# Optimization experiments

Measured on AMD Instinct MI355X. Metric: run time of the kernel, lower is better.

Reference implementation:

```python
import jax, jax.numpy as jnp
import numpy as np

B, L, D, DIN, S, R, K = 2, 1024, 1024, 2048, 16, 64, 4


def setup_inputs() -> dict:
    key = jax.random.key(0)
    ks = jax.random.split(key, 8)
    f = lambda k, sh, sc: jax.random.normal(k, sh, jnp.float32) * sc
    return {
        "x": f(ks[0], (B, L, D), 1.0),
        "norm_w": jnp.ones((D,), jnp.float32),
        "W_in": f(ks[1], (D, 2 * DIN), D ** -0.5),
        "conv_w": f(ks[2], (DIN, 1, K), 0.5),
        "conv_b": jnp.zeros((DIN,), jnp.float32),
        "W_x": f(ks[3], (DIN, R + 2 * S), DIN ** -0.5),
        "W_dt": f(ks[4], (R, DIN), R ** -0.5),
        "b_dt": f(ks[5], (DIN,), 0.1),
        "A_log": jnp.log(jnp.broadcast_to(jnp.arange(1, S + 1, dtype=jnp.float32), (DIN, S))),
        "D_skip": jnp.ones((DIN,), jnp.float32),
        "W_out": f(ks[6], (DIN, D), DIN ** -0.5),
    }


def reference(x, norm_w, W_in, conv_w, conv_b, W_x, W_dt, b_dt, A_log, D_skip, W_out):
    eps = 1e-5
    # RMSNorm
    xn = x * jax.lax.rsqrt(jnp.mean(x * x, axis=-1, keepdims=True) + eps) * norm_w
    # input projection -> (x_branch, gate)
    xz = xn @ W_in                       # [B,L,2*DIN]
    xi, z = jnp.split(xz, 2, axis=-1)
    # causal depthwise conv1d along L
    xt = jnp.transpose(xi, (0, 2, 1))    # [B,DIN,L]
    xc = jax.lax.conv_general_dilated(xt, conv_w, (1,), [(K - 1, 0)],
                                      feature_group_count=DIN)
    xc = jnp.transpose(xc, (0, 2, 1)) + conv_b
    xc = jax.nn.silu(xc)                 # [B,L,DIN]
    # input-dependent SSM parameters
    xd = xc @ W_x                        # [B,L,R+2S]
    dt, Bm, Cm = jnp.split(xd, [R, R + S], axis=-1)
    dt = jax.nn.softplus(dt @ W_dt + b_dt)           # [B,L,DIN]
    A = -jnp.exp(A_log)                              # [DIN,S]
    dA = jnp.exp(dt[..., None] * A)                  # [B,L,DIN,S]
    dBu = (dt * xc)[..., None] * Bm[:, :, None, :]   # [B,L,DIN,S]
    # selective scan: h_t = dA_t * h_{t-1} + dBu_t (parallel associative scan)
    def comb(c1, c2):
        a1, b1 = c1
        a2, b2 = c2
        return a1 * a2, a2 * b1 + b2
    _, h = jax.lax.associative_scan(comb, (dA, dBu), axis=1)
    y = jnp.einsum('blds,bls->bld', h, Cm) + D_skip * xc
    y = y * jax.nn.silu(z)
    return x + y @ W_out
```

## Files before the change

### kernel.cpp

```cpp
#include <hip/hip_runtime.h>

#define B_    2
#define L_    1024
#define D_    1024
#define DIN_  2048
#define S_    16
#define R_    64
#define NTOK  (B_ * L_)
#define NCH   32
#define LC    (L_ / NCH)

typedef unsigned short u16;
typedef short bf16x8 __attribute__((ext_vector_type(8)));
typedef float f32x4  __attribute__((ext_vector_type(4)));

__device__ __forceinline__ u16 f2bf(float f) {
    union { float f; unsigned u; } v; v.f = f;
    return (u16)((v.u + 0x7FFFu + ((v.u >> 16) & 1u)) >> 16);
}
__device__ __forceinline__ float bf2f(u16 b) {
    union { unsigned u; float f; } v; v.u = (unsigned)b << 16;
    return v.f;
}

__global__ __launch_bounds__(256) void rmsnorm_kernel(
    const float* __restrict__ x, const float* __restrict__ w, u16* __restrict__ xn) {
    int row = blockIdx.x;
    const float4 v = ((const float4*)(x + (size_t)row * D_))[threadIdx.x];
    float ss = v.x * v.x + v.y * v.y + v.z * v.z + v.w * v.w;
#pragma unroll
    for (int o = 32; o > 0; o >>= 1) ss += __shfl_down(ss, o);
    __shared__ float red[4];
    if ((threadIdx.x & 63) == 0) red[threadIdx.x >> 6] = ss;
    __syncthreads();
    float tot = red[0] + red[1] + red[2] + red[3];
    float sc = rsqrtf(tot * (1.f / (float)D_) + 1e-5f);
    const float4 wv = ((const float4*)w)[threadIdx.x];
    ushort4 o;
    o.x = f2bf(v.x * sc * wv.x);
    o.y = f2bf(v.y * sc * wv.y);
    o.z = f2bf(v.z * sc * wv.z);
    o.w = f2bf(v.w * sc * wv.w);
    ((ushort4*)(xn + (size_t)row * D_))[threadIdx.x] = o;
}

__device__ __forceinline__ void transp_tile(
    const float* __restrict__ src, u16* __restrict__ dst,
    int R, int Csrc, int cx, int cy, int tx, int ty) {
    __shared__ float tile[32][33];
    int c0 = cx * 32, r0 = cy * 32;
#pragma unroll
    for (int i = 0; i < 32; i += 8)
        tile[ty + i][tx] = (c0 + tx < Csrc)
            ? src[(size_t)(r0 + ty + i) * Csrc + c0 + tx] : 0.f;
    __syncthreads();
#pragma unroll
    for (int i = 0; i < 32; i += 8)
        dst[(size_t)(c0 + ty + i) * R + r0 + tx] = f2bf(tile[tx][ty + i]);
}

__global__ __launch_bounds__(256) void transpose_all_kernel(
    const float* __restrict__ W_in,  u16* __restrict__ WinT,
    const float* __restrict__ W_out, u16* __restrict__ WoutT,
    const float* __restrict__ W_x,   u16* __restrict__ WxT,
    const float* __restrict__ W_dt,  u16* __restrict__ WdtT) {
    int bid = blockIdx.x;
    int tx = threadIdx.x & 31, ty = threadIdx.x >> 5;
    if (bid < 4096) {
        transp_tile(W_in, WinT, D_, 2 * DIN_, bid % 128, bid / 128, tx, ty);
    } else if (bid < 6144) {
        int b = bid - 4096;
        transp_tile(W_out, WoutT, DIN_, D_, b % 32, b / 32, tx, ty);
    } else if (bid < 6400) {
        int b = bid - 6144;
        transp_tile(W_x, WxT, DIN_, 96, b % 4, b / 4, tx, ty);
    } else {
        int b = bid - 6400;
        transp_tile(W_dt, WdtT, R_, DIN_, b % 64, b / 64, tx, ty);
    }
}

#define BK 64
template<int BM, int BN>
__global__ __launch_bounds__(256) void gemm_bf16(
    const u16* __restrict__ A, int lda,
    const u16* __restrict__ Bt, int ldb,
    float* __restrict__ C, u16* __restrict__ Cbf, int ldc,
    const float* __restrict__ aux,
    int M, int N, int K, int mode) {
    constexpr int WGM = (BM >= 128) ? 2 : 1;
    constexpr int WGN = 4 / WGM;
    constexpr int FM = BM / (16 * WGM);
    constexpr int FN = BN / (16 * WGN);
    constexpr int ABYTES = BM * BK * 2;
    constexpr int BBYTES = BN * BK * 2;
    __shared__ __align__(16) u16 As[2][BM * BK];
    __shared__ __align__(16) u16 Bs[2][BN * BK];
    const int t = threadIdx.x;
    const int w = t >> 6;
    const int l = t & 63;
    const int lr = l & 15;
    const int kg = l >> 4;
    const int wm = (w / WGN) * (BM / WGM);
    const int wn = (w % WGN) * (BN / WGN);

    int nwg = gridDim.x * gridDim.y * gridDim.z;
    int flat = blockIdx.x + gridDim.x * (blockIdx.y + gridDim.y * blockIdx.z);
    int swz = (flat & 7) * (nwg >> 3) + (flat >> 3);
    int bx = swz % gridDim.x;
    int rem = swz / gridDim.x;
    int by = rem % gridDim.y;
    int bz = rem / gridDim.y;

    const int row0 = by * BM;
    const int col0 = bx * BN;
    const int kbase = bz * K;

    auto stage = [&](int buf, int k0) {
#pragma unroll
        for (int i = 0; i < ABYTES; i += 4096) {
            int off = i + t * 16;
            int grow = off >> 7;
            int sw = ((off >> 4) & 7) ^ (grow & 7);
            const u16* ga = A + (size_t)(row0 + grow) * lda + k0 + sw * 8;
            __builtin_amdgcn_global_load_lds(
                (const __attribute__((address_space(1))) unsigned int*)(const void*)ga,
                (__attribute__((address_space(3))) unsigned int*)(void*)&As[buf][off >> 1],
                16, 0, 0);
        }
#pragma unroll
        for (int i = 0; i < BBYTES; i += 4096) {
            int off = i + t * 16;
            int grow = off >> 7;
            int sw = ((off >> 4) & 7) ^ (grow & 7);
            const u16* gb = Bt + (size_t)(col0 + grow) * ldb + k0 + sw * 8;
            __builtin_amdgcn_global_load_lds(
                (const __attribute__((address_space(1))) unsigned int*)(const void*)gb,
                (__attribute__((address_space(3))) unsigned int*)(void*)&Bs[buf][off >> 1],
                16, 0, 0);
        }
    };

    f32x4 acc[FM][FN];
#pragma unroll
    for (int i = 0; i < FM; ++i)
#pragma unroll
        for (int j = 0; j < FN; ++j) acc[i][j] = (f32x4){0.f, 0.f, 0.f, 0.f};

    const int nt = K / BK;
    stage(0, kbase);
    asm volatile("s_waitcnt vmcnt(0)" ::: "memory");
    __builtin_amdgcn_s_barrier();
    asm volatile("" ::: "memory");

    int cur = 0;
    for (int tt = 0; tt < nt; ++tt) {
        if (tt + 1 < nt) stage(cur ^ 1, kbase + (tt + 1) * BK);
#pragma unroll
        for (int ks = 0; ks < 2; ++ks) {
            bf16x8 af[FM], bfr[FN];
#pragma unroll
            for (int mt = 0; mt < FM; ++mt) {
                int ar = wm + mt * 16 + lr;
                af[mt] = *(const bf16x8*)&As[cur][ar * 64 + (((ks << 2) | kg) ^ (ar & 7)) * 8];
            }
#pragma unroll
            for (int nt2 = 0; nt2 < FN; ++nt2) {
                int br = wn + nt2 * 16 + lr;
                bfr[nt2] = *(const bf16x8*)&Bs[cur][br * 64 + (((ks << 2) | kg) ^ (br & 7)) * 8];
            }
            __builtin_amdgcn_s_setprio(1);
#pragma unroll
            for (int mt = 0; mt < FM; ++mt)
#pragma unroll
                for (int nt2 = 0; nt2 < FN; ++nt2)
                    acc[mt][nt2] = __builtin_amdgcn_mfma_f32_16x16x32_bf16(
                        af[mt], bfr[nt2], acc[mt][nt2], 0, 0, 0);
            __builtin_amdgcn_s_setprio(0);
        }
        if (tt + 1 < nt) {
            asm volatile("s_waitcnt vmcnt(0)" ::: "memory");
            __builtin_amdgcn_s_barrier();
            asm volatile("" ::: "memory");
        }
        cur ^= 1;
    }

    size_t pbase = (mode == 3) ? (size_t)bz * M * N : 0;
#pragma unroll
    for (int mt = 0; mt < FM; ++mt) {
#pragma unroll
        for (int nt2 = 0; nt2 < FN; ++nt2) {
#pragma unroll
            for (int r = 0; r < 4; ++r) {
                int row = row0 + wm + mt * 16 + kg * 4 + r;
                int col = col0 + wn + nt2 * 16 + lr;
                float v = acc[mt][nt2][r];
                if (mode == 1) { v += aux[col]; v = (v > 20.f) ? v : log1pf(__expf(v)); }
                else if (mode == 2) { v += aux[(size_t)row * ldc + col]; }
                if (C)   C[pbase + (size_t)row * ldc + col] = v;
                if (Cbf) Cbf[(size_t)row * ldc + col] = f2bf(v);
            }
        }
    }
}

__global__ __launch_bounds__(256) void reduce_wx_kernel(
    const float* __restrict__ part, float* __restrict__ xd, u16* __restrict__ xdb) {
    int i = blockIdx.x * 256 + threadIdx.x;
    float4 s = ((const float4*)part)[i];
#pragma unroll
    for (int k = 1; k < 16; ++k) {
        float4 v = ((const float4*)(part + (size_t)k * NTOK * 128))[i];
        s.x += v.x; s.y += v.y; s.z += v.z; s.w += v.w;
    }
    ((float4*)xd)[i] = s;
    ushort4 o; o.x = f2bf(s.x); o.y = f2bf(s.y); o.z = f2bf(s.z); o.w = f2bf(s.w);
    ((ushort4*)xdb)[i] = o;
}

__global__ __launch_bounds__(256) void reduce_out_kernel(
    const float* __restrict__ part, const float* __restrict__ x, float* __restrict__ out) {
    int i = blockIdx.x * 256 + threadIdx.x;
    float4 s = ((const float4*)part)[i];
#pragma unroll
    for (int k = 1; k < 4; ++k) {
        float4 v = ((const float4*)(part + (size_t)k * NTOK * D_))[i];
        s.x += v.x; s.y += v.y; s.z += v.z; s.w += v.w;
    }
    float4 xv = ((const float4*)x)[i];
    s.x += xv.x; s.y += xv.y; s.z += xv.z; s.w += xv.w;
    ((float4*)out)[i] = s;
}

__global__ __launch_bounds__(256) void conv_silu_kernel(
    const float* __restrict__ xz, const float* __restrict__ cw,
    const float* __restrict__ cb, u16* __restrict__ xcb) {
    size_t idx = (size_t)blockIdx.x * 256 + threadIdx.x;
    int c = (int)(idx & (DIN_ - 1));
    int g = (int)(idx >> 11);
    int bl0 = g * 4;
    int l0 = bl0 & (L_ - 1);
    const float4 w = ((const float4*)cw)[c];
    float bias = cb[c];
    float v[7];
#pragma unroll
    for (int k = 0; k < 7; ++k) {
        int off = k - 3;
        v[k] = (l0 + off >= 0) ? xz[(size_t)(bl0 + off) * 4096 + c] : 0.f;
    }
#pragma unroll
    for (int j = 0; j < 4; ++j) {
        float acc = bias + v[j] * w.x + v[j + 1] * w.y + v[j + 2] * w.z + v[j + 3] * w.w;
        float s = acc / (1.f + __expf(-acc));
        xcb[(size_t)(bl0 + j) * DIN_ + c] = f2bf(s);
    }
}

__global__ __launch_bounds__(256) void scan_chunk_kernel(
    const float* __restrict__ dt, const u16* __restrict__ xcb,
    const float* __restrict__ xd, const float* __restrict__ A_log,
    float* __restrict__ Pout, float* __restrict__ Hout) {
    int din = blockIdx.x * 256 + threadIdx.x;
    int c = blockIdx.y, b = blockIdx.z;
    float a[S_], h[S_];
#pragma unroll
    for (int q = 0; q < 4; ++q) {
        float4 av = ((const float4*)(A_log + (size_t)din * S_))[q];
        a[q * 4 + 0] = -__expf(av.x); a[q * 4 + 1] = -__expf(av.y);
        a[q * 4 + 2] = -__expf(av.z); a[q * 4 + 3] = -__expf(av.w);
    }
#pragma unroll
    for (int s = 0; s < S_; ++s) h[s] = 0.f;
    float sdt = 0.f;
    size_t rbase = (size_t)b * L_ + (size_t)c * LC;
#pragma unroll 2
    for (int i = 0; i < LC; ++i) {
        size_t row = rbase + i;
        float dtv = dt[row * DIN_ + din];
        float xcv = bf2f(xcb[row * DIN_ + din]);
        float du = dtv * xcv;
        sdt += dtv;
        const float4* bp = (const float4*)(xd + row * 128 + 64);
        float4 B0 = bp[0], B1 = bp[1], B2 = bp[2], B3 = bp[3];
        float Bv[S_] = {B0.x, B0.y, B0.z, B0.w, B1.x, B1.y, B1.z, B1.w,
                        B2.x, B2.y, B2.z, B2.w, B3.x, B3.y, B3.z, B3.w};
#pragma unroll
        for (int s = 0; s < S_; ++s) {
            float dA = __expf(dtv * a[s]);
            h[s] = h[s] * dA + du * Bv[s];
        }
    }
    size_t obase = ((size_t)(b * NCH + c) * DIN_ + din) * S_;
#pragma unroll
    for (int q = 0; q < 4; ++q) {
        float4 pv, hv;
        pv.x = __expf(a[q * 4 + 0] * sdt); pv.y = __expf(a[q * 4 + 1] * sdt);
        pv.z = __expf(a[q * 4 + 2] * sdt); pv.w = __expf(a[q * 4 + 3] * sdt);
        hv.x = h[q * 4 + 0]; hv.y = h[q * 4 + 1]; hv.z = h[q * 4 + 2]; hv.w = h[q * 4 + 3];
        ((float4*)(Pout + obase))[q] = pv;
        ((float4*)(Hout + obase))[q] = hv;
    }
}

__global__ __launch_bounds__(256) void scan_combine_kernel(
    const float* __restrict__ P, const float* __restrict__ H,
    float* __restrict__ h0) {
    int tid = blockIdx.x * 256 + threadIdx.x;
    int ds = tid & (DIN_ * S_ - 1);
    int b = tid >> 15;
    float h = 0.f;
#pragma unroll
    for (int c = 0; c < NCH; ++c) {
        size_t idx = ((size_t)(b * NCH + c) * DIN_ * S_) + ds;
        h0[idx] = h;
        h = H[idx] + P[idx] * h;
    }
}

__global__ __launch_bounds__(256) void scan_final_kernel(
    const float* __restrict__ dt, const u16* __restrict__ xcb,
    const float* __restrict__ xd, const float* __restrict__ A_log,
    const float* __restrict__ h0, const float* __restrict__ Dskip,
    const float* __restrict__ xz, u16* __restrict__ yg) {
    int din = blockIdx.x * 256 + threadIdx.x;
    int c = blockIdx.y, b = blockIdx.z;
    float a[S_], h[S_];
#pragma unroll
    for (int q = 0; q < 4; ++q) {
        float4 av = ((const float4*)(A_log + (size_t)din * S_))[q];
        a[q * 4 + 0] = -__expf(av.x); a[q * 4 + 1] = -__expf(av.y);
        a[q * 4 + 2] = -__expf(av.z); a[q * 4 + 3] = -__expf(av.w);
    }
    size_t ibase = ((size_t)(b * NCH + c) * DIN_ + din) * S_;
#pragma unroll
    for (int q = 0; q < 4; ++q) {
        float4 hv = ((const float4*)(h0 + ibase))[q];
        h[q * 4 + 0] = hv.x; h[q * 4 + 1] = hv.y; h[q * 4 + 2] = hv.z; h[q * 4 + 3] = hv.w;
    }
    float dsk = Dskip[din];
    size_t rbase = (size_t)b * L_ + (size_t)c * LC;
#pragma unroll 2
    for (int i = 0; i < LC; ++i) {
        size_t row = rbase + i;
        float dtv = dt[row * DIN_ + din];
        float xcv = bf2f(xcb[row * DIN_ + din]);
        float du = dtv * xcv;
        const float4* bp = (const float4*)(xd + row * 128 + 64);
        float4 B0 = bp[0], B1 = bp[1], B2 = bp[2], B3 = bp[3];
        const float4* cp = (const float4*)(xd + row * 128 + 80);
        float4 C0 = cp[0], C1 = cp[1], C2 = cp[2], C3 = cp[3];
        float Bv[S_] = {B0.x, B0.y, B0.z, B0.w, B1.x, B1.y, B1.z, B1.w,
                        B2.x, B2.y, B2.z, B2.w, B3.x, B3.y, B3.z, B3.w};
        float Cv[S_] = {C0.x, C0.y, C0.z, C0.w, C1.x, C1.y, C1.z, C1.w,
                        C2.x, C2.y, C2.z, C2.w, C3.x, C3.y, C3.z, C3.w};
        float py = 0.f;
#pragma unroll
        for (int s = 0; s < S_; ++s) {
            float dA = __expf(dtv * a[s]);
            h[s] = h[s] * dA + du * Bv[s];
            py += h[s] * Cv[s];
        }
        float zv = xz[row * 4096 + DIN_ + din];
        float y = (py + dsk * xcv) * (zv / (1.f + __expf(-zv)));
        yg[row * DIN_ + din] = f2bf(y);
    }
}

extern "C" void kernel_launch(void* const* d_in, const int* in_sizes, int n_in,
                              void* d_out, int out_size, void* d_ws, size_t ws_size,
                              hipStream_t stream) {
    const float* x      = (const float*)d_in[0];
    const float* norm_w = (const float*)d_in[1];
    const float* W_in   = (const float*)d_in[2];
    const float* conv_w = (const float*)d_in[3];
    const float* conv_b = (const float*)d_in[4];
    const float* W_x    = (const float*)d_in[5];
    const float* W_dt   = (const float*)d_in[6];
    const float* b_dt   = (const float*)d_in[7];
    const float* A_log  = (const float*)d_in[8];
    const float* D_skip = (const float*)d_in[9];
    const float* W_out  = (const float*)d_in[10];
    float* out = (float*)d_out;

    char* p = (char*)d_ws;
    auto alloc = [&](size_t bytes) {
        char* r = p;
        p += (bytes + 255) & ~(size_t)255;
        return r;
    };
    u16*   xn    = (u16*)alloc((size_t)NTOK * D_ * 2);
    u16*   WinT  = (u16*)alloc((size_t)2 * DIN_ * D_ * 2);
    u16*   WoutT = (u16*)alloc((size_t)D_ * DIN_ * 2);
    u16*   WxT   = (u16*)alloc((size_t)128 * DIN_ * 2);
    u16*   WdtT  = (u16*)alloc((size_t)DIN_ * R_ * 2);
    float* xz    = (float*)alloc((size_t)NTOK * 2 * DIN_ * 4);
    u16*   xcb   = (u16*)alloc((size_t)NTOK * DIN_ * 2);
    float* xd    = (float*)alloc((size_t)NTOK * 128 * 4);
    u16*   xdb   = (u16*)alloc((size_t)NTOK * 128 * 2);
    float* dtb   = (float*)alloc((size_t)NTOK * DIN_ * 4);
    u16*   yg    = (u16*)alloc((size_t)NTOK * DIN_ * 2);
    float* Pbuf  = (float*)alloc((size_t)B_ * NCH * DIN_ * S_ * 4);
    float* Hbuf  = (float*)alloc((size_t)B_ * NCH * DIN_ * S_ * 4);
    float* h0buf = (float*)alloc((size_t)B_ * NCH * DIN_ * S_ * 4);

    float* part_wx  = dtb;
    float* part_out = xz;

    rmsnorm_kernel<<<NTOK, 256, 0, stream>>>(x, norm_w, xn);
    transpose_all_kernel<<<6528, 256, 0, stream>>>(
        W_in, WinT, W_out, WoutT, W_x, WxT, W_dt, WdtT);

    gemm_bf16<64, 128><<<dim3(2 * DIN_ / 128, NTOK / 64), 256, 0, stream>>>(
        xn, D_, WinT, D_, xz, nullptr, 2 * DIN_, nullptr, NTOK, 2 * DIN_, D_, 0);
    conv_silu_kernel<<<(NTOK * DIN_ / 4) / 256, 256, 0, stream>>>(xz, conv_w, conv_b, xcb);
    gemm_bf16<64, 128><<<dim3(1, NTOK / 64, 16), 256, 0, stream>>>(
        xcb, DIN_, WxT, DIN_, part_wx, nullptr, 128, nullptr, NTOK, 128, DIN_ / 16, 3);
    reduce_wx_kernel<<<(NTOK * 128 / 4) / 256, 256, 0, stream>>>(part_wx, xd, xdb);
    gemm_bf16<64, 128><<<dim3(DIN_ / 128, NTOK / 64), 256, 0, stream>>>(
        xdb, 128, WdtT, R_, dtb, nullptr, DIN_, b_dt, NTOK, DIN_, R_, 1);
    {
        dim3 grid(DIN_ / 256, NCH, B_);
        scan_chunk_kernel<<<grid, 256, 0, stream>>>(dtb, xcb, xd, A_log, Pbuf, Hbuf);
        scan_combine_kernel<<<(B_ * DIN_ * S_) / 256, 256, 0, stream>>>(Pbuf, Hbuf, h0buf);
        scan_final_kernel<<<grid, 256, 0, stream>>>(dtb, xcb, xd, A_log, h0buf, D_skip, xz, yg);
    }
    gemm_bf16<64, 128><<<dim3(D_ / 128, NTOK / 64, 4), 256, 0, stream>>>(
        yg, DIN_, WoutT, DIN_, part_out, nullptr, D_, nullptr, NTOK, D_, DIN_ / 4, 3);
    reduce_out_kernel<<<(NTOK * D_ / 4) / 256, 256, 0, stream>>>(part_out, x, out);
}
```

Measured before the change: 187.0 us.

## Halve GEMM K-tile to 32 and remap workgroups into XCD-local column blocks

Shrinks the GEMM K tile from 64 to 32, with a matching 4-way XOR LDS swizzle and one MFMA k-step per stage. It also replaces the simple XCD round-robin swizzle with a mapping that gives each XCD a contiguous group of CX column tiles and a range of rows, for better L2 reuse of B tiles. The smaller tile halves LDS use, which may raise occupancy. In exchange it doubles the number of barrier and wait iterations and halves the work per pipeline stage.

Measured after the change: 178.7 us. -4.5%, faster.

```diff
diff --git a/kernel.cpp b/kernel.cpp
--- a/kernel.cpp
+++ b/kernel.cpp
@@ -80,8 +80,8 @@
     }
 }
 
-#define BK 64
-template<int BM, int BN>
+#define BK 32
+template<int BM, int BN, int CX>
 __global__ __launch_bounds__(256) void gemm_bf16(
     const u16* __restrict__ A, int lda,
     const u16* __restrict__ Bt, int ldb,
@@ -104,13 +104,16 @@
     const int wm = (w / WGN) * (BM / WGM);
     const int wn = (w % WGN) * (BN / WGN);
 
-    int nwg = gridDim.x * gridDim.y * gridDim.z;
-    int flat = blockIdx.x + gridDim.x * (blockIdx.y + gridDim.y * blockIdx.z);
-    int swz = (flat & 7) * (nwg >> 3) + (flat >> 3);
-    int bx = swz % gridDim.x;
-    int rem = swz / gridDim.x;
-    int by = rem % gridDim.y;
-    int bz = rem / gridDim.y;
+    const int GX = gridDim.x, GY = gridDim.y;
+    int h = blockIdx.x + GX * (blockIdx.y + GY * blockIdx.z);
+    int xcd = h & 7, pos = h >> 3;
+    int ncx = GX / CX;
+    int chunk = (GX * GY * gridDim.z) >> 3;
+    int rpc = chunk / CX;
+    int bx = (xcd % ncx) * CX + pos % CX;
+    int r  = (xcd / ncx) * rpc + pos / CX;
+    int by = r % GY;
+    int bz = r / GY;
 
     const int row0 = by * BM;
     const int col0 = bx * BN;
@@ -120,8 +123,8 @@
 #pragma unroll
         for (int i = 0; i < ABYTES; i += 4096) {
             int off = i + t * 16;
-            int grow = off >> 7;
-            int sw = ((off >> 4) & 7) ^ (grow & 7);
+            int grow = off >> 6;
+            int sw = ((off >> 4) & 3) ^ ((grow >> 1) & 3);
             const u16* ga = A + (size_t)(row0 + grow) * lda + k0 + sw * 8;
             __builtin_amdgcn_global_load_lds(
                 (const __attribute__((address_space(1))) unsigned int*)(const void*)ga,
@@ -131,8 +134,8 @@
 #pragma unroll
         for (int i = 0; i < BBYTES; i += 4096) {
             int off = i + t * 16;
-            int grow = off >> 7;
-            int sw = ((off >> 4) & 7) ^ (grow & 7);
+            int grow = off >> 6;
+            int sw = ((off >> 4) & 3) ^ ((grow >> 1) & 3);
             const u16* gb = Bt + (size_t)(col0 + grow) * ldb + k0 + sw * 8;
             __builtin_amdgcn_global_load_lds(
                 (const __attribute__((address_space(1))) unsigned int*)(const void*)gb,
@@ -156,28 +159,25 @@
     int cur = 0;
     for (int tt = 0; tt < nt; ++tt) {
         if (tt + 1 < nt) stage(cur ^ 1, kbase + (tt + 1) * BK);
-#pragma unroll
-        for (int ks = 0; ks < 2; ++ks) {
-            bf16x8 af[FM], bfr[FN];
-#pragma unroll
-            for (int mt = 0; mt < FM; ++mt) {
-                int ar = wm + mt * 16 + lr;
-                af[mt] = *(const bf16x8*)&As[cur][ar * 64 + (((ks << 2) | kg) ^ (ar & 7)) * 8];
-            }
-#pragma unroll
-            for (int nt2 = 0; nt2 < FN; ++nt2) {
-                int br = wn + nt2 * 16 + lr;
-                bfr[nt2] = *(const bf16x8*)&Bs[cur][br * 64 + (((ks << 2) | kg) ^ (br & 7)) * 8];
-            }
-            __builtin_amdgcn_s_setprio(1);
-#pragma unroll
-            for (int mt = 0; mt < FM; ++mt)
-#pragma unroll
-                for (int nt2 = 0; nt2 < FN; ++nt2)
-                    acc[mt][nt2] = __builtin_amdgcn_mfma_f32_16x16x32_bf16(
-                        af[mt], bfr[nt2], acc[mt][nt2], 0, 0, 0);
-            __builtin_amdgcn_s_setprio(0);
-        }
+        bf16x8 af[FM], bfr[FN];
+#pragma unroll
+        for (int mt = 0; mt < FM; ++mt) {
+            int ar = wm + mt * 16 + lr;
+            af[mt] = *(const bf16x8*)&As[cur][ar * 32 + (kg ^ ((ar >> 1) & 3)) * 8];
+        }
+#pragma unroll
+        for (int nt2 = 0; nt2 < FN; ++nt2) {
+            int br = wn + nt2 * 16 + lr;
+            bfr[nt2] = *(const bf16x8*)&Bs[cur][br * 32 + (kg ^ ((br >> 1) & 3)) * 8];
+        }
+        __builtin_amdgcn_s_setprio(1);
+#pragma unroll
+        for (int mt = 0; mt < FM; ++mt)
+#pragma unroll
+            for (int nt2 = 0; nt2 < FN; ++nt2)
+                acc[mt][nt2] = __builtin_amdgcn_mfma_f32_16x16x32_bf16(
+                    af[mt], bfr[nt2], acc[mt][nt2], 0, 0, 0);
+        __builtin_amdgcn_s_setprio(0);
         if (tt + 1 < nt) {
             asm volatile("s_waitcnt vmcnt(0)" ::: "memory");
             __builtin_amdgcn_s_barrier();
@@ -192,10 +192,10 @@
 #pragma unroll
         for (int nt2 = 0; nt2 < FN; ++nt2) {
 #pragma unroll
-            for (int r = 0; r < 4; ++r) {
-                int row = row0 + wm + mt * 16 + kg * 4 + r;
+            for (int r2 = 0; r2 < 4; ++r2) {
+                int row = row0 + wm + mt * 16 + kg * 4 + r2;
                 int col = col0 + wn + nt2 * 16 + lr;
-                float v = acc[mt][nt2][r];
+                float v = acc[mt][nt2][r2];
                 if (mode == 1) { v += aux[col]; v = (v > 20.f) ? v : log1pf(__expf(v)); }
                 else if (mode == 2) { v += aux[(size_t)row * ldc + col]; }
                 if (C)   C[pbase + (size_t)row * ldc + col] = v;
@@ -411,13 +411,13 @@
     transpose_all_kernel<<<6528, 256, 0, stream>>>(
         W_in, WinT, W_out, WoutT, W_x, WxT, W_dt, WdtT);
 
-    gemm_bf16<64, 128><<<dim3(2 * DIN_ / 128, NTOK / 64), 256, 0, stream>>>(
+    gemm_bf16<64, 128, 8><<<dim3(2 * DIN_ / 128, NTOK / 64), 256, 0, stream>>>(
         xn, D_, WinT, D_, xz, nullptr, 2 * DIN_, nullptr, NTOK, 2 * DIN_, D_, 0);
     conv_silu_kernel<<<(NTOK * DIN_ / 4) / 256, 256, 0, stream>>>(xz, conv_w, conv_b, xcb);
-    gemm_bf16<64, 128><<<dim3(1, NTOK / 64, 16), 256, 0, stream>>>(
+    gemm_bf16<64, 128, 1><<<dim3(1, NTOK / 64, 16), 256, 0, stream>>>(
         xcb, DIN_, WxT, DIN_, part_wx, nullptr, 128, nullptr, NTOK, 128, DIN_ / 16, 3);
     reduce_wx_kernel<<<(NTOK * 128 / 4) / 256, 256, 0, stream>>>(part_wx, xd, xdb);
-    gemm_bf16<64, 128><<<dim3(DIN_ / 128, NTOK / 64), 256, 0, stream>>>(
+    gemm_bf16<64, 128, 8><<<dim3(DIN_ / 128, NTOK / 64), 256, 0, stream>>>(
         xdb, 128, WdtT, R_, dtb, nullptr, DIN_, b_dt, NTOK, DIN_, R_, 1);
     {
         dim3 grid(DIN_ / 256, NCH, B_);
@@ -425,7 +425,7 @@
         scan_combine_kernel<<<(B_ * DIN_ * S_) / 256, 256, 0, stream>>>(Pbuf, Hbuf, h0buf);
         scan_final_kernel<<<grid, 256, 0, stream>>>(dtb, xcb, xd, A_log, h0buf, D_skip, xz, yg);
     }
-    gemm_bf16<64, 128><<<dim3(D_ / 128, NTOK / 64, 4), 256, 0, stream>>>(
+    gemm_bf16<64, 128, 8><<<dim3(D_ / 128, NTOK / 64, 4), 256, 0, stream>>>(
         yg, DIN_, WoutT, DIN_, part_out, nullptr, D_, nullptr, NTOK, D_, DIN_ / 4, 3);
     reduce_out_kernel<<<(NTOK * D_ / 4) / 256, 256, 0, stream>>>(part_out, x, out);
 }
```
